# Kernel optimization log

Hardware: AMD Instinct MI355X
Metric: run time of the kernel (lower is better)

The kernel has to match this reference:

```python
import jax, jax.numpy as jnp
import numpy as np

B, N, D = 128, 131072, 1

def setup_inputs() -> dict:
    key = jax.random.key(0)
    k1, k2, k3, k4, k5 = jax.random.split(key, 5)
    particles = jax.random.normal(k1, (B, N, D), dtype=jnp.float32)
    particle_weights = jax.random.uniform(k2, (B, N), dtype=jnp.float32)
    observation = jax.random.normal(k3, (B, 1), dtype=jnp.float32)
    noise = jax.random.normal(k4, (B, N, D), dtype=jnp.float32)  # std-normal; scaled by sqrt(10) inside
    uniforms = jax.random.uniform(k5, (B, N), dtype=jnp.float32)
    return {
        "particles": particles,
        "particle_weights": particle_weights,
        "observation": observation,
        "noise": noise,
        "uniforms": uniforms,
        "timestep_number": 3,
    }

def _resample(particles, particle_weights, uniforms):
    # Efficient equivalent of the original O(B*N^2) tile + argmax(cumsum >= u):
    # first index where cumsum >= u  ==  searchsorted(cumsum, u, side='left').
    cum = jnp.cumsum(particle_weights, axis=-1)            # [B, N]
    idx = jax.vmap(lambda c, u: jnp.searchsorted(c, u, side='left'))(cum, uniforms)  # [B, N]
    resampled = jnp.take_along_axis(particles, idx[..., None], axis=1)  # [B, N, D]
    n = particles.shape[1]
    resampled_w = jnp.full(particle_weights.shape, 1.0 / n, dtype=particle_weights.dtype)
    return resampled, resampled_w

def reference(particles, particle_weights, observation, noise, uniforms, timestep_number):
    # Note: the original forward calls resample_particles but then builds the
    # transition from the ORIGINAL particles; resampled values never reach the
    # outputs. We keep the call for fidelity (XLA will DCE it).
    _resampled, _rw = _resample(particles, particle_weights, uniforms)

    # UNGM transition: x/2 + 25*x/(x^2+1) + 8*cos(1.2*t) + N(0, 10)
    mean = particles / 2.0 + 25.0 * (particles / (particles ** 2 + 1.0))
    mean = mean + 8.0 * jnp.cos(1.2 * jnp.float32(timestep_number))
    new_particles = mean + noise * np.float32(np.sqrt(10.0))   # [B, N, 1]

    # Observation likelihood: y ~ N(x^2/20, 1)
    obs_mean = (new_particles ** 2 / 20.0)[..., 0]             # [B, N]
    log_prob = -0.5 * (observation - obs_mean) ** 2 - 0.5 * np.float32(np.log(2.0 * np.pi))
    w = particle_weights * jnp.exp(log_prob)                   # [B, N]
    w = w / jnp.sum(w, axis=1, keepdims=True)
    return new_particles, w
```

## Files before the change

kernel.cpp:

```cpp
#include <hip/hip_runtime.h>
#include <math.h>

#define PF_B 128
#define PF_N 131072
#define TPB 256
#define EPT 8
#define EPB (TPB * EPT)
#define BLOCKS_PER_BATCH (PF_N / EPB)

typedef float v4f __attribute__((ext_vector_type(4)));


__global__ __launch_bounds__(TPB) void pf_compute(
    const float* __restrict__ particles,
    const float* __restrict__ weights,
    const float* __restrict__ obs,
    const float* __restrict__ noise,
    const int*   __restrict__ tstep,
    float* __restrict__ np_out,
    float* __restrict__ w_out,
    float* __restrict__ sums)
{
    const int b     = blockIdx.x / BLOCKS_PER_BATCH;
    const int chunk = blockIdx.x % BLOCKS_PER_BATCH;
    const long base = (long)b * PF_N + (long)chunk * EPB;

    const float ob     = obs[b];
    const float c      = 8.0f * cosf(1.2f * (float)(*tstep));
    const float sq10   = 3.16227770f;
    const float nhl2pi = -0.9189385f;

    float lsum = 0.0f;

    #pragma unroll
    for (int k = 0; k < EPT / 4; ++k) {
        const long idx = base + (long)k * (TPB * 4) + (long)threadIdx.x * 4;
        const v4f x4  = __builtin_nontemporal_load((const v4f*)(particles + idx));
        const v4f n4  = __builtin_nontemporal_load((const v4f*)(noise + idx));
        const v4f wt4 = __builtin_nontemporal_load((const v4f*)(weights + idx));

        v4f xn, wn;

        #pragma unroll
        for (int j = 0; j < 4; ++j) {
            const float x = x4[j];
            const float mean = x * 0.5f + 25.0f * (x / (x * x + 1.0f)) + c;
            const float xnew = mean + n4[j] * sq10;
            xn[j] = xnew;
            const float om = (xnew * xnew) / 20.0f;
            const float d  = ob - om;
            const float lp = -0.5f * d * d + nhl2pi;
            const float wv = wt4[j] * __expf(lp);
            wn[j] = wv;
            lsum += wv;
        }

        __builtin_nontemporal_store(xn, (v4f*)(np_out + idx));
        *(v4f*)(w_out + idx) = wn;
    }

    #pragma unroll
    for (int off = 32; off > 0; off >>= 1)
        lsum += __shfl_down(lsum, off, 64);

    __shared__ float red[TPB / 64];
    if ((threadIdx.x & 63) == 0) red[threadIdx.x >> 6] = lsum;
    __syncthreads();
    if (threadIdx.x == 0) {
        float s = 0.0f;
        #pragma unroll
        for (int i = 0; i < TPB / 64; ++i) s += red[i];
        atomicAdd(&sums[b], s);
    }
}

__global__ __launch_bounds__(TPB) void pf_normalize(
    float* __restrict__ w_out,
    const float* __restrict__ sums)
{
    const int b     = blockIdx.x / BLOCKS_PER_BATCH;
    const int chunk = blockIdx.x % BLOCKS_PER_BATCH;
    const long base = (long)b * PF_N + (long)chunk * EPB;
    const float inv = 1.0f / sums[b];

    #pragma unroll
    for (int k = 0; k < EPT / 4; ++k) {
        const long idx = base + (long)k * (TPB * 4) + (long)threadIdx.x * 4;
        v4f v = *(const v4f*)(w_out + idx);
        v *= inv;
        __builtin_nontemporal_store(v, (v4f*)(w_out + idx));
    }
}

extern "C" void kernel_launch(void* const* d_in, const int* in_sizes, int n_in,
                              void* d_out, int out_size, void* d_ws, size_t ws_size,
                              hipStream_t stream) {
    const float* particles = (const float*)d_in[0];
    const float* weights   = (const float*)d_in[1];
    const float* obs       = (const float*)d_in[2];
    const float* noise     = (const float*)d_in[3];
    const int*   tstep     = (const int*)d_in[5];

    float* np_out = (float*)d_out;
    float* w_out  = (float*)d_out + (long)PF_B * PF_N;
    float* sums   = (float*)d_ws;

    hipMemsetAsync(d_ws, 0, PF_B * sizeof(float), stream);

    const int grid = PF_B * BLOCKS_PER_BATCH;
    pf_compute<<<grid, TPB, 0, stream>>>(particles, weights, obs, noise, tstep,
                                         np_out, w_out, sums);
    pf_normalize<<<grid, TPB, 0, stream>>>(w_out, sums);
}
```

Baseline: 326.4 us.

## Recompute weights in a second pass instead of writing and rereading unnormalized weights

The first kernel now only computes per-block partial sums of the unnormalized weights and writes them to workspace, without storing any outputs. The second kernel reads the inputs again, recomputes the transition and likelihood, reduces the 64 partials per batch with a wavefront shuffle, and writes the normalized weights and new particles once. This removes the intermediate write and reread of the weight array, the memset and the atomics. In exchange the three input arrays are read twice. The first pass drops the nontemporal loads, likely so those inputs can stay in the large last-level cache for the second read.

```diff
diff --git a/kernel.cpp b/kernel.cpp
--- a/kernel.cpp
+++ b/kernel.cpp
@@ -11,52 +11,47 @@
 typedef float v4f __attribute__((ext_vector_type(4)));
 
 
-__global__ __launch_bounds__(TPB) void pf_compute(
+__device__ __forceinline__ void compute_elem(
+    float x, float n, float wt, float c, float ob,
+    float& xnew, float& wv)
+{
+    const float mean = x * 0.5f + 25.0f * (x / (x * x + 1.0f)) + c;
+    xnew = mean + n * 3.16227770f;
+    const float om = (xnew * xnew) / 20.0f;
+    const float d  = ob - om;
+    const float lp = -0.5f * d * d + (-0.9189385f);
+    wv = wt * __expf(lp);
+}
+
+__global__ __launch_bounds__(TPB) void pf_sum(
     const float* __restrict__ particles,
     const float* __restrict__ weights,
     const float* __restrict__ obs,
     const float* __restrict__ noise,
     const int*   __restrict__ tstep,
-    float* __restrict__ np_out,
-    float* __restrict__ w_out,
-    float* __restrict__ sums)
+    float* __restrict__ partials)
 {
     const int b     = blockIdx.x / BLOCKS_PER_BATCH;
     const int chunk = blockIdx.x % BLOCKS_PER_BATCH;
     const long base = (long)b * PF_N + (long)chunk * EPB;
 
-    const float ob     = obs[b];
-    const float c      = 8.0f * cosf(1.2f * (float)(*tstep));
-    const float sq10   = 3.16227770f;
-    const float nhl2pi = -0.9189385f;
+    const float ob = obs[b];
+    const float c  = 8.0f * cosf(1.2f * (float)(*tstep));
 
     float lsum = 0.0f;
 
     #pragma unroll
     for (int k = 0; k < EPT / 4; ++k) {
         const long idx = base + (long)k * (TPB * 4) + (long)threadIdx.x * 4;
-        const v4f x4  = __builtin_nontemporal_load((const v4f*)(particles + idx));
-        const v4f n4  = __builtin_nontemporal_load((const v4f*)(noise + idx));
-        const v4f wt4 = __builtin_nontemporal_load((const v4f*)(weights + idx));
-
-        v4f xn, wn;
-
+        const v4f x4  = *(const v4f*)(particles + idx);
+        const v4f n4  = *(const v4f*)(noise + idx);
+        const v4f wt4 = *(const v4f*)(weights + idx);
         #pragma unroll
         for (int j = 0; j < 4; ++j) {
-            const float x = x4[j];
-            const float mean = x * 0.5f + 25.0f * (x / (x * x + 1.0f)) + c;
-            const float xnew = mean + n4[j] * sq10;
-            xn[j] = xnew;
-            const float om = (xnew * xnew) / 20.0f;
-            const float d  = ob - om;
-            const float lp = -0.5f * d * d + nhl2pi;
-            const float wv = wt4[j] * __expf(lp);
-            wn[j] = wv;
+            float xn, wv;
+            compute_elem(x4[j], n4[j], wt4[j], c, ob, xn, wv);
             lsum += wv;
         }
-
-        __builtin_nontemporal_store(xn, (v4f*)(np_out + idx));
-        *(v4f*)(w_out + idx) = wn;
     }
 
     #pragma unroll
@@ -70,25 +65,52 @@
         float s = 0.0f;
         #pragma unroll
         for (int i = 0; i < TPB / 64; ++i) s += red[i];
-        atomicAdd(&sums[b], s);
+        partials[blockIdx.x] = s;
     }
 }
 
-__global__ __launch_bounds__(TPB) void pf_normalize(
-    float* __restrict__ w_out,
-    const float* __restrict__ sums)
+__global__ __launch_bounds__(TPB) void pf_final(
+    const float* __restrict__ particles,
+    const float* __restrict__ weights,
+    const float* __restrict__ obs,
+    const float* __restrict__ noise,
+    const int*   __restrict__ tstep,
+    const float* __restrict__ partials,
+    float* __restrict__ np_out,
+    float* __restrict__ w_out)
 {
     const int b     = blockIdx.x / BLOCKS_PER_BATCH;
     const int chunk = blockIdx.x % BLOCKS_PER_BATCH;
     const long base = (long)b * PF_N + (long)chunk * EPB;
-    const float inv = 1.0f / sums[b];
+
+    const float ob = obs[b];
+    const float c  = 8.0f * cosf(1.2f * (float)(*tstep));
+
+    const int lane = threadIdx.x & 63;
+    float p = partials[b * BLOCKS_PER_BATCH + lane];
+    #pragma unroll
+    for (int off = 32; off > 0; off >>= 1)
+        p += __shfl_xor(p, off, 64);
+    const float inv = 1.0f / p;
 
     #pragma unroll
     for (int k = 0; k < EPT / 4; ++k) {
         const long idx = base + (long)k * (TPB * 4) + (long)threadIdx.x * 4;
-        v4f v = *(const v4f*)(w_out + idx);
-        v *= inv;
-        __builtin_nontemporal_store(v, (v4f*)(w_out + idx));
+        const v4f x4  = *(const v4f*)(particles + idx);
+        const v4f n4  = *(const v4f*)(noise + idx);
+        const v4f wt4 = *(const v4f*)(weights + idx);
+
+        v4f xn, wn;
+        #pragma unroll
+        for (int j = 0; j < 4; ++j) {
+            float xnew, wv;
+            compute_elem(x4[j], n4[j], wt4[j], c, ob, xnew, wv);
+            xn[j] = xnew;
+            wn[j] = wv * inv;
+        }
+
+        __builtin_nontemporal_store(xn, (v4f*)(np_out + idx));
+        __builtin_nontemporal_store(wn, (v4f*)(w_out + idx));
     }
 }
 
@@ -101,14 +123,13 @@
     const float* noise     = (const float*)d_in[3];
     const int*   tstep     = (const int*)d_in[5];
 
-    float* np_out = (float*)d_out;
-    float* w_out  = (float*)d_out + (long)PF_B * PF_N;
-    float* sums   = (float*)d_ws;
-
-    hipMemsetAsync(d_ws, 0, PF_B * sizeof(float), stream);
+    float* np_out   = (float*)d_out;
+    float* w_out    = (float*)d_out + (long)PF_B * PF_N;
+    float* partials = (float*)d_ws;
 
     const int grid = PF_B * BLOCKS_PER_BATCH;
-    pf_compute<<<grid, TPB, 0, stream>>>(particles, weights, obs, noise, tstep,
-                                         np_out, w_out, sums);
-    pf_normalize<<<grid, TPB, 0, stream>>>(w_out, sums);
+    pf_sum<<<grid, TPB, 0, stream>>>(particles, weights, obs, noise, tstep,
+                                     partials);
+    pf_final<<<grid, TPB, 0, stream>>>(particles, weights, obs, noise, tstep,
+                                       partials, np_out, w_out);
 }
```

Result: no change. 332.6 us (+1.9%).
